# Kernel tuning notes

Measured on AMD Instinct MI355X. Metric: run time of the kernel, lower is better.

Reference implementation:

```python
import jax, jax.numpy as jnp
import numpy as np

N = 50000        # nodes
E = 800000       # edges (avg degree 16)
G = 64           # graphs in batch
F_IN = 9
OUT = 10


def setup_inputs() -> dict:
    key = jax.random.key(0)
    ks = jax.random.split(key, 20)
    def w(k, fi, fo):
        return jax.random.normal(k, (fi, fo), dtype=jnp.float32) * (1.0 / np.sqrt(fi))
    inp = {
        "x": jax.random.normal(ks[0], (N, F_IN), dtype=jnp.float32),
        "edge_index": jax.random.randint(ks[1], (2, E), 0, N, dtype=jnp.int64),
        "batch": jnp.sort(jax.random.randint(ks[2], (N,), 0, G, dtype=jnp.int64)),
        # GCNConv weights (PyG: x @ W then normalized scatter-add, + bias)
        "W1": w(ks[3], F_IN, 128), "b1": jnp.zeros((128,), jnp.float32),
        "W2": w(ks[4], 128, 256),  "b2": jnp.zeros((256,), jnp.float32),
        "W3": w(ks[5], 256, 256),  "b3": jnp.zeros((256,), jnp.float32),
        "W4": w(ks[6], 256, 256),  "b4": jnp.zeros((256,), jnp.float32),
        # dense head
        "Wl2": w(ks[7], 256, 128), "bl2": jnp.zeros((128,), jnp.float32),
        "Wl3": w(ks[8], 128, 128), "bl3": jnp.zeros((128,), jnp.float32),
        "Wl":  w(ks[9], 128, OUT), "bl":  jnp.zeros((OUT,), jnp.float32),
    }
    return inp


def reference(x, edge_index, batch, W1, b1, W2, b2, W3, b3, W4, b4,
              Wl2, bl2, Wl3, bl3, Wl, bl):
    # GCNConv with self-loops and symmetric deg^{-1/2} normalization
    loops = jnp.arange(N, dtype=edge_index.dtype)
    src = jnp.concatenate([edge_index[0], loops])   # [E+N]
    dst = jnp.concatenate([edge_index[1], loops])
    deg = jax.ops.segment_sum(jnp.ones_like(src, dtype=x.dtype), dst, num_segments=N)
    dinv = jax.lax.rsqrt(deg)                        # deg >= 1 due to self-loops
    norm = (dinv[src] * dinv[dst])[:, None]          # [E+N, 1]

    def conv(h, W, b):
        msg = (h @ W)[src] * norm                    # gather + normalize
        return jax.ops.segment_sum(msg, dst, num_segments=N) + b

    h = jax.nn.relu(conv(x, W1, b1))
    h = jax.nn.relu(conv(h, W2, b2))
    h = jax.nn.relu(conv(h, W3, b3))
    h = conv(h, W4, b4)                              # no relu before pool
    g = jax.ops.segment_max(h, batch, num_segments=G)  # global_max_pool -> [G, 256]
    g = jax.nn.relu(g @ Wl2 + bl2)
    g = jax.nn.relu(g @ Wl3 + bl3)
    out = g @ Wl + bl                                # [G, OUT]
    return jnp.squeeze(out)
```

## Files before the change

### kernel.cpp

```cpp
#include <hip/hip_runtime.h>
#include <float.h>

#define NN 50000
#define NE 800000
#define NG 64
#define CAP 64

typedef __attribute__((ext_vector_type(8))) _Float16 f16x8;
typedef __attribute__((ext_vector_type(4))) float f32x4;
typedef __attribute__((ext_vector_type(4))) _Float16 half4;
typedef __attribute__((ext_vector_type(2))) _Float16 half2v;
typedef unsigned int u32;

__device__ __forceinline__ unsigned f2mono(float f) {
  unsigned b = __float_as_uint(f);
  return (b & 0x80000000u) ? ~b : (b | 0x80000000u);
}
__device__ __forceinline__ float mono2f(unsigned u) {
  unsigned b = (u & 0x80000000u) ? (u & 0x7fffffffu) : ~u;
  return __uint_as_float(b);
}
__device__ __forceinline__ void gl_lds16(const void* g, void* l) {
  __builtin_amdgcn_global_load_lds((const __attribute__((address_space(1))) u32*)g,
                                   (__attribute__((address_space(3))) u32*)l, 16, 0, 0);
}

#define CGRID 782
#define CSTRIDE (CGRID * 256)
__global__ void k_count(const int* __restrict__ src, const int* __restrict__ dst,
                        int* __restrict__ cnt, int* __restrict__ col) {
  int idx = blockIdx.x * 256 + threadIdx.x;
#pragma unroll
  for (int k = 0; k < 4; ++k) {
    int e = idx + k * CSTRIDE;
    if (e < NE) {
      int d = dst[e];
      int s = src[e];
      if ((unsigned)d < NN && (unsigned)s < NN) {
        int pos = atomicAdd(&cnt[d], 1);
        if (pos < CAP) col[d * CAP + pos] = s;
      }
    }
  }
}

__global__ void k_dinv(const int* __restrict__ cnt, float* __restrict__ dinv,
                       const float* __restrict__ x, float* __restrict__ xs) {
  int v = blockIdx.x * blockDim.x + threadIdx.x;
  if (v >= NN) return;
  float d = rsqrtf((float)cnt[v] + 1.0f);
  dinv[v] = d;
#pragma unroll
  for (int i = 0; i < 9; ++i) xs[v * 9 + i] = x[v * 9 + i] * d;
}

__device__ __forceinline__ void splitw1(const float* W, _Float16* Wh, _Float16* Wl,
                                        int i, int K, int Nc) {
  int k = i / Nc, n = i - k * Nc;
  float w = W[i];
  _Float16 h = (_Float16)w;
  _Float16 l = (_Float16)(w - (float)h);
  Wh[(size_t)n * K + k] = h;
  Wl[(size_t)n * K + k] = l;
}
__global__ void k_splitw3(const float* __restrict__ W2, const float* __restrict__ W3,
                          const float* __restrict__ W4,
                          _Float16* __restrict__ W2h, _Float16* __restrict__ W2l,
                          _Float16* __restrict__ W3h, _Float16* __restrict__ W3l,
                          _Float16* __restrict__ W4h, _Float16* __restrict__ W4l) {
  int i = blockIdx.x * 256 + threadIdx.x;
  const int n2 = 128 * 256, n3 = 256 * 256;
  if (i < n2) splitw1(W2, W2h, W2l, i, 128, 256);
  else if (i < n2 + n3) splitw1(W3, W3h, W3l, i - n2, 256, 256);
  else if (i < n2 + 2 * n3) splitw1(W4, W4h, W4l, i - n2 - n3, 256, 256);
}

__global__ __launch_bounds__(256) void k_agg9(const float* __restrict__ xs,
                                              float* __restrict__ out,
                                              const int* __restrict__ cnt,
                                              const int* __restrict__ col,
                                              const float* __restrict__ dinv) {
  int v = (blockIdx.x * 256 + threadIdx.x) >> 4;
  int l = threadIdx.x & 15;
  if (v >= NN) return;
  int c = cnt[v]; if (c > CAP) c = CAP;
  const int* cl = col + v * CAP;
  float acc = (l < 9) ? xs[v * 9 + l] : 0.0f;
  int j = 0;
  for (; j + 4 <= c; j += 4) {
    int4 u = *(const int4*)(cl + j);
    float a0 = (l < 9) ? xs[u.x * 9 + l] : 0.f;
    float a1 = (l < 9) ? xs[u.y * 9 + l] : 0.f;
    float a2 = (l < 9) ? xs[u.z * 9 + l] : 0.f;
    float a3 = (l < 9) ? xs[u.w * 9 + l] : 0.f;
    acc += (a0 + a1) + (a2 + a3);
  }
  for (; j < c; ++j) {
    int u = cl[j];
    if (l < 9) acc += xs[u * 9 + l];
  }
  if (l < 9) out[v * 9 + l] = acc * dinv[v];
}

__global__ __launch_bounds__(256) void k_gemm9(const float* __restrict__ in,
                                               const float* __restrict__ W,
                                               const float* __restrict__ bias,
                                               const float* __restrict__ dinv,
                                               _Float16* __restrict__ out) {
  __shared__ float sW[9 * 128];
  __shared__ float sb[128];
  int t = threadIdx.x;
  if (t < 128) sb[t] = bias[t];
  for (int i = t; i < 9 * 128; i += 256) sW[i] = W[i];
  __syncthreads();
  int r = blockIdx.x * 2 + (t >> 7);
  int c = t & 127;
  if (r >= NN) return;
  float acc = sb[c];
#pragma unroll
  for (int i = 0; i < 9; ++i) acc += in[r * 9 + i] * sW[i * 128 + c];
  out[r * 128 + c] = (_Float16)(fmaxf(acc, 0.0f) * dinv[r]);
}

__global__ __launch_bounds__(256) void k_agg128(const half2v* __restrict__ h,
                                                half2v* __restrict__ out,
                                                const int* __restrict__ cnt,
                                                const int* __restrict__ col,
                                                const float* __restrict__ dinv) {
  int gw = (blockIdx.x * 256 + threadIdx.x) >> 6;
  int lane = threadIdx.x & 63;
  int w0 = gw * 2, w1 = w0 + 1;
  if (w0 >= NN) return;
  half2v s0 = h[(size_t)w0 * 64 + lane];
  half2v s1 = h[(size_t)w1 * 64 + lane];
  float a0x = (float)s0.x, a0y = (float)s0.y;
  float a1x = (float)s1.x, a1y = (float)s1.y;
  int c0 = cnt[w0]; if (c0 > CAP) c0 = CAP;
  int c1 = cnt[w1]; if (c1 > CAP) c1 = CAP;
  const int* cl0 = col + (size_t)w0 * CAP;
  const int* cl1 = col + (size_t)w1 * CAP;
  int j0 = 0, j1 = 0;
  while (j0 + 4 <= c0 && j1 + 4 <= c1) {
    int4 u0 = *(const int4*)(cl0 + j0);
    int4 u1 = *(const int4*)(cl1 + j1);
    half2v t00 = h[(size_t)u0.x * 64 + lane];
    half2v t01 = h[(size_t)u0.y * 64 + lane];
    half2v t02 = h[(size_t)u0.z * 64 + lane];
    half2v t03 = h[(size_t)u0.w * 64 + lane];
    half2v t10 = h[(size_t)u1.x * 64 + lane];
    half2v t11 = h[(size_t)u1.y * 64 + lane];
    half2v t12 = h[(size_t)u1.z * 64 + lane];
    half2v t13 = h[(size_t)u1.w * 64 + lane];
    a0x += ((float)t00.x + (float)t01.x) + ((float)t02.x + (float)t03.x);
    a0y += ((float)t00.y + (float)t01.y) + ((float)t02.y + (float)t03.y);
    a1x += ((float)t10.x + (float)t11.x) + ((float)t12.x + (float)t13.x);
    a1y += ((float)t10.y + (float)t11.y) + ((float)t12.y + (float)t13.y);
    j0 += 4; j1 += 4;
  }
  for (; j0 + 4 <= c0; j0 += 4) {
    int4 u = *(const int4*)(cl0 + j0);
    half2v t0 = h[(size_t)u.x * 64 + lane];
    half2v t1 = h[(size_t)u.y * 64 + lane];
    half2v t2 = h[(size_t)u.z * 64 + lane];
    half2v t3 = h[(size_t)u.w * 64 + lane];
    a0x += ((float)t0.x + (float)t1.x) + ((float)t2.x + (float)t3.x);
    a0y += ((float)t0.y + (float)t1.y) + ((float)t2.y + (float)t3.y);
  }
  for (; j1 + 4 <= c1; j1 += 4) {
    int4 u = *(const int4*)(cl1 + j1);
    half2v t0 = h[(size_t)u.x * 64 + lane];
    half2v t1 = h[(size_t)u.y * 64 + lane];
    half2v t2 = h[(size_t)u.z * 64 + lane];
    half2v t3 = h[(size_t)u.w * 64 + lane];
    a1x += ((float)t0.x + (float)t1.x) + ((float)t2.x + (float)t3.x);
    a1y += ((float)t0.y + (float)t1.y) + ((float)t2.y + (float)t3.y);
  }
  for (; j0 < c0; ++j0) {
    half2v tv = h[(size_t)cl0[j0] * 64 + lane];
    a0x += (float)tv.x; a0y += (float)tv.y;
  }
  for (; j1 < c1; ++j1) {
    half2v tv = h[(size_t)cl1[j1] * 64 + lane];
    a1x += (float)tv.x; a1y += (float)tv.y;
  }
  float d0 = dinv[w0], d1 = dinv[w1];
  half2v o0, o1;
  o0.x = (_Float16)(a0x * d0); o0.y = (_Float16)(a0y * d0);
  o1.x = (_Float16)(a1x * d1); o1.y = (_Float16)(a1y * d1);
  out[(size_t)w0 * 64 + lane] = o0;
  out[(size_t)w1 * 64 + lane] = o1;
}

__global__ __launch_bounds__(256) void k_agg256(const half4* __restrict__ h,
                                                half4* __restrict__ out,
                                                const int* __restrict__ cnt,
                                                const int* __restrict__ col,
                                                const float* __restrict__ dinv) {
  int gw = (blockIdx.x * 256 + threadIdx.x) >> 6;
  int lane = threadIdx.x & 63;
  int w0 = gw * 2, w1 = w0 + 1;
  if (w0 >= NN) return;
  half4 s0 = h[(size_t)w0 * 64 + lane];
  half4 s1 = h[(size_t)w1 * 64 + lane];
  float a0x = (float)s0.x, a0y = (float)s0.y, a0z = (float)s0.z, a0w = (float)s0.w;
  float a1x = (float)s1.x, a1y = (float)s1.y, a1z = (float)s1.z, a1w = (float)s1.w;
  int c0 = cnt[w0]; if (c0 > CAP) c0 = CAP;
  int c1 = cnt[w1]; if (c1 > CAP) c1 = CAP;
  const int* cl0 = col + (size_t)w0 * CAP;
  const int* cl1 = col + (size_t)w1 * CAP;
  int j0 = 0, j1 = 0;
  while (j0 + 4 <= c0 && j1 + 4 <= c1) {
    int4 u0 = *(const int4*)(cl0 + j0);
    int4 u1 = *(const int4*)(cl1 + j1);
    half4 t00 = h[(size_t)u0.x * 64 + lane];
    half4 t01 = h[(size_t)u0.y * 64 + lane];
    half4 t02 = h[(size_t)u0.z * 64 + lane];
    half4 t03 = h[(size_t)u0.w * 64 + lane];
    half4 t10 = h[(size_t)u1.x * 64 + lane];
    half4 t11 = h[(size_t)u1.y * 64 + lane];
    half4 t12 = h[(size_t)u1.z * 64 + lane];
    half4 t13 = h[(size_t)u1.w * 64 + lane];
    a0x += ((float)t00.x + (float)t01.x) + ((float)t02.x + (float)t03.x);
    a0y += ((float)t00.y + (float)t01.y) + ((float)t02.y + (float)t03.y);
    a0z += ((float)t00.z + (float)t01.z) + ((float)t02.z + (float)t03.z);
    a0w += ((float)t00.w + (float)t01.w) + ((float)t02.w + (float)t03.w);
    a1x += ((float)t10.x + (float)t11.x) + ((float)t12.x + (float)t13.x);
    a1y += ((float)t10.y + (float)t11.y) + ((float)t12.y + (float)t13.y);
    a1z += ((float)t10.z + (float)t11.z) + ((float)t12.z + (float)t13.z);
    a1w += ((float)t10.w + (float)t11.w) + ((float)t12.w + (float)t13.w);
    j0 += 4; j1 += 4;
  }
  for (; j0 + 4 <= c0; j0 += 4) {
    int4 u = *(const int4*)(cl0 + j0);
    half4 t0 = h[(size_t)u.x * 64 + lane];
    half4 t1 = h[(size_t)u.y * 64 + lane];
    half4 t2 = h[(size_t)u.z * 64 + lane];
    half4 t3 = h[(size_t)u.w * 64 + lane];
    a0x += ((float)t0.x + (float)t1.x) + ((float)t2.x + (float)t3.x);
    a0y += ((float)t0.y + (float)t1.y) + ((float)t2.y + (float)t3.y);
    a0z += ((float)t0.z + (float)t1.z) + ((float)t2.z + (float)t3.z);
    a0w += ((float)t0.w + (float)t1.w) + ((float)t2.w + (float)t3.w);
  }
  for (; j1 + 4 <= c1; j1 += 4) {
    int4 u = *(const int4*)(cl1 + j1);
    half4 t0 = h[(size_t)u.x * 64 + lane];
    half4 t1 = h[(size_t)u.y * 64 + lane];
    half4 t2 = h[(size_t)u.z * 64 + lane];
    half4 t3 = h[(size_t)u.w * 64 + lane];
    a1x += ((float)t0.x + (float)t1.x) + ((float)t2.x + (float)t3.x);
    a1y += ((float)t0.y + (float)t1.y) + ((float)t2.y + (float)t3.y);
    a1z += ((float)t0.z + (float)t1.z) + ((float)t2.z + (float)t3.z);
    a1w += ((float)t0.w + (float)t1.w) + ((float)t2.w + (float)t3.w);
  }
  for (; j0 < c0; ++j0) {
    half4 tv = h[(size_t)cl0[j0] * 64 + lane];
    a0x += (float)tv.x; a0y += (float)tv.y; a0z += (float)tv.z; a0w += (float)tv.w;
  }
  for (; j1 < c1; ++j1) {
    half4 tv = h[(size_t)cl1[j1] * 64 + lane];
    a1x += (float)tv.x; a1y += (float)tv.y; a1z += (float)tv.z; a1w += (float)tv.w;
  }
  float d0 = dinv[w0], d1 = dinv[w1];
  half4 o0, o1;
  o0.x = (_Float16)(a0x * d0); o0.y = (_Float16)(a0y * d0);
  o0.z = (_Float16)(a0z * d0); o0.w = (_Float16)(a0w * d0);
  o1.x = (_Float16)(a1x * d1); o1.y = (_Float16)(a1y * d1);
  o1.z = (_Float16)(a1z * d1); o1.w = (_Float16)(a1w * d1);
  out[(size_t)w0 * 64 + lane] = o0;
  out[(size_t)w1 * 64 + lane] = o1;
}

__global__ __launch_bounds__(256) void k_mm(const _Float16* __restrict__ A,
                                            const _Float16* __restrict__ Bh,
                                            const _Float16* __restrict__ Bl,
                                            const float* __restrict__ bias,
                                            _Float16* __restrict__ C,
                                            const float* __restrict__ dinv,
                                            const int* __restrict__ batch,
                                            unsigned* __restrict__ gpool,
                                            int M, int K, int Nc, int mode) {
  __shared__ __align__(16) _Float16 Alds[128 * 64];
  __shared__ __align__(16) _Float16 Bhl[128 * 64];
  __shared__ __align__(16) _Float16 Bll[128 * 64];
  int t = threadIdx.x;
  int wave = t >> 6, lane = t & 63;
  int wm = wave & 1, wn = wave >> 1;
  int rowBase = blockIdx.x * 128;
  int colBase = blockIdx.y * 128;
  int lm = lane & 15;
  int q  = lane >> 4;

  int srl = wave * 32 + (lane >> 3);
  int sj  = lane & 7;
  int ssw = lane >> 3;
  int gseg = sj ^ ssw;

  f32x4 acc[4][4];
#pragma unroll
  for (int i = 0; i < 4; ++i)
#pragma unroll
    for (int j = 0; j < 4; ++j) acc[i][j] = (f32x4){0.f, 0.f, 0.f, 0.f};

  int nit = K >> 6;
  for (int it = 0; it < nit; ++it) {
    __syncthreads();
#pragma unroll
    for (int c = 0; c < 4; ++c) {
      int rl = srl + c * 8;
      int ga = rowBase + rl; if (ga > M - 1) ga = M - 1;
      int gb = colBase + rl;
      unsigned off = (unsigned)it * 64 + gseg * 8;
      int ldst = (wave * 32 + c * 8) * 64 + lane * 8;
      gl_lds16(A  + (size_t)ga * K + off, Alds + ldst);
      gl_lds16(Bh + (size_t)gb * K + off, Bhl + ldst);
      gl_lds16(Bl + (size_t)gb * K + off, Bll + ldst);
    }
    __syncthreads();

#pragma unroll
    for (int s2 = 0; s2 < 2; ++s2) {
      int slotq = ((s2 << 2) | q);
      f16x8 vbh[4], vbl[4];
#pragma unroll
      for (int ni = 0; ni < 4; ++ni) {
        int rB = wn * 64 + ni * 16 + lm;
        int slot = slotq ^ (lm & 7);
        vbh[ni] = *(const f16x8*)(Bhl + rB * 64 + slot * 8);
        vbl[ni] = *(const f16x8*)(Bll + rB * 64 + slot * 8);
      }
#pragma unroll
      for (int mi = 0; mi < 4; ++mi) {
        int rA = wm * 64 + mi * 16 + lm;
        int slot = slotq ^ (lm & 7);
        f16x8 va = *(const f16x8*)(Alds + rA * 64 + slot * 8);
#pragma unroll
        for (int ni = 0; ni < 4; ++ni) {
          acc[mi][ni] = __builtin_amdgcn_mfma_f32_16x16x32_f16(va, vbh[ni], acc[mi][ni], 0, 0, 0);
          acc[mi][ni] = __builtin_amdgcn_mfma_f32_16x16x32_f16(va, vbl[ni], acc[mi][ni], 0, 0, 0);
        }
      }
    }
  }

  int rowOff = (lane >> 4) * 4;
  if (mode == 2) {
    __syncthreads();
    unsigned* ldsPool = (unsigned*)Alds;
    for (int i = t; i < 4 * 256; i += 256) ldsPool[i] = 0u;
    __syncthreads();
    int b0 = batch[rowBase];
#pragma unroll
    for (int mi = 0; mi < 4; ++mi) {
#pragma unroll
      for (int ni = 0; ni < 4; ++ni) {
        int gc = colBase + wn * 64 + ni * 16 + lm;
        float bsv = bias[gc];
#pragma unroll
        for (int r = 0; r < 4; ++r) {
          int gr = rowBase + wm * 64 + mi * 16 + rowOff + r;
          if (gr < M) {
            float v = acc[mi][ni][r] + bsv;
            int idx = batch[gr] - b0;
            if (idx < 0) idx = 0;
            if (idx > 3) idx = 3;
            atomicMax(&ldsPool[idx * 256 + gc], f2mono(v));
          }
        }
      }
    }
    __syncthreads();
#pragma unroll
    for (int s4 = 0; s4 < 4; ++s4) {
      unsigned mv = ldsPool[s4 * 256 + t];
      int gb = b0 + s4;
      if (mv && gb < NG) atomicMax(&gpool[gb * 256 + t], mv);
    }
  } else {
#pragma unroll
    for (int mi = 0; mi < 4; ++mi) {
#pragma unroll
      for (int ni = 0; ni < 4; ++ni) {
        int gc = colBase + wn * 64 + ni * 16 + lm;
        float bsv = bias[gc];
#pragma unroll
        for (int r = 0; r < 4; ++r) {
          int gr = rowBase + wm * 64 + mi * 16 + rowOff + r;
          if (gr < M) {
            float v = fmaxf(acc[mi][ni][r] + bsv, 0.0f);
            C[(size_t)gr * Nc + gc] = (_Float16)(v * dinv[gr]);
          }
        }
      }
    }
  }
}

__global__ __launch_bounds__(256) void k_head(const unsigned* __restrict__ g,
                                              const float* __restrict__ Wl2, const float* __restrict__ bl2,
                                              const float* __restrict__ Wl3, const float* __restrict__ bl3,
                                              const float* __restrict__ Wl, const float* __restrict__ bl,
                                              float* __restrict__ out) {
  __shared__ float s0[256];
  __shared__ float s1[128];
  __shared__ float s2[128];
  int b = blockIdx.x, t = threadIdx.x;
  s0[t] = mono2f(g[b * 256 + t]);
  __syncthreads();
  if (t < 128) {
    float acc = bl2[t];
    for (int k = 0; k < 256; ++k) acc += s0[k] * Wl2[k * 128 + t];
    s1[t] = fmaxf(acc, 0.0f);
  }
  __syncthreads();
  if (t < 128) {
    float acc = bl3[t];
    for (int k = 0; k < 128; ++k) acc += s1[k] * Wl3[k * 128 + t];
    s2[t] = fmaxf(acc, 0.0f);
  }
  __syncthreads();
  if (t < 10) {
    float acc = bl[t];
    for (int k = 0; k < 128; ++k) acc += s2[k] * Wl[k * 10 + t];
    out[b * 10 + t] = acc;
  }
}

extern "C" void kernel_launch(void* const* d_in, const int* in_sizes, int n_in,
                              void* d_out, int out_size, void* d_ws, size_t ws_size,
                              hipStream_t stream) {
  const float* x   = (const float*)d_in[0];
  const int* eidx  = (const int*)d_in[1];
  const int* batch = (const int*)d_in[2];
  const float* W1 = (const float*)d_in[3];   const float* b1 = (const float*)d_in[4];
  const float* W2 = (const float*)d_in[5];   const float* b2 = (const float*)d_in[6];
  const float* W3 = (const float*)d_in[7];   const float* b3 = (const float*)d_in[8];
  const float* W4 = (const float*)d_in[9];   const float* b4 = (const float*)d_in[10];
  const float* Wl2 = (const float*)d_in[11]; const float* bl2 = (const float*)d_in[12];
  const float* Wl3 = (const float*)d_in[13]; const float* bl3 = (const float*)d_in[14];
  const float* Wl  = (const float*)d_in[15]; const float* bl  = (const float*)d_in[16];
  float* out = (float*)d_out;

  _Float16* bufA = (_Float16*)d_ws;
  _Float16* bufB = bufA + (size_t)NN * 256;
  int* cnt  = (int*)(bufB + (size_t)NN * 256);
  float* dinv = (float*)(cnt + NN);
  int* col  = (int*)(dinv + NN);
  unsigned* g = (unsigned*)(col + (size_t)NN * CAP);
  _Float16* W2h = (_Float16*)(g + NG * 256);
  _Float16* W2l = W2h + 256 * 128;
  _Float16* W3h = W2l + 256 * 128;
  _Float16* W3l = W3h + 256 * 256;
  _Float16* W4h = W3l + 256 * 256;
  _Float16* W4l = W4h + 256 * 256;
  float* xs = (float*)bufA;
  float* agg9out = (float*)bufB;

  const int* src = eidx;
  const int* dst = eidx + NE;

  hipMemsetAsync(cnt, 0, NN * sizeof(int), stream);
  hipMemsetAsync(g, 0, NG * 256 * sizeof(unsigned), stream);

  k_count<<<CGRID, 256, 0, stream>>>(src, dst, cnt, col);
  k_dinv<<<(NN + 255) / 256, 256, 0, stream>>>(cnt, dinv, x, xs);

  k_splitw3<<<(128 * 256 + 2 * 256 * 256 + 255) / 256, 256, 0, stream>>>(
      W2, W3, W4, W2h, W2l, W3h, W3l, W4h, W4l);

  k_agg9<<<(NN + 15) / 16, 256, 0, stream>>>(xs, agg9out, cnt, col, dinv);
  k_gemm9<<<NN / 2, 256, 0, stream>>>(agg9out, W1, b1, dinv, bufA);

  dim3 gmm((NN + 127) / 128, 2);
  int aggGrid = ((NN / 2) * 64 + 255) / 256;

  k_agg128<<<aggGrid, 256, 0, stream>>>((const half2v*)bufA, (half2v*)bufB, cnt, col, dinv);
  k_mm<<<gmm, 256, 0, stream>>>(bufB, W2h, W2l, b2, bufA, dinv, batch, g, NN, 128, 256, 1);

  k_agg256<<<aggGrid, 256, 0, stream>>>((const half4*)bufA, (half4*)bufB, cnt, col, dinv);
  k_mm<<<gmm, 256, 0, stream>>>(bufB, W3h, W3l, b3, bufA, dinv, batch, g, NN, 256, 256, 1);

  k_agg256<<<aggGrid, 256, 0, stream>>>((const half4*)bufA, (half4*)bufB, cnt, col, dinv);
  k_mm<<<gmm, 256, 0, stream>>>(bufB, W4h, W4l, b4, bufA, dinv, batch, g, NN, 256, 256, 2);

  k_head<<<NG, 256, 0, stream>>>(g, Wl2, bl2, Wl3, bl3, Wl, bl, out);
}
```

Measured before the change: 458.1 us.

## Store adjacency indices as u16, remap GEMM block order, fold pool memset

Neighbor indices in the padded adjacency table are stored as 16-bit values instead of 32-bit, halving index traffic in every aggregation kernel. The count kernel switches to one edge per thread, the pooled-max buffer is zeroed inside k_dinv instead of by a separate memset, and the GEMM uses a 1-D grid remapped so that both column tiles of a row block run next to each other for better A-tile reuse in cache. Node ids go up to 49999, so they fit in u16, but the tail loops that still read cl[j] now read u16 values, so the change relies on that fitting.

```diff
diff --git a/kernel.cpp b/kernel.cpp
--- a/kernel.cpp
+++ b/kernel.cpp
@@ -11,6 +11,7 @@
 typedef __attribute__((ext_vector_type(4))) _Float16 half4;
 typedef __attribute__((ext_vector_type(2))) _Float16 half2v;
 typedef unsigned int u32;
+typedef unsigned short u16;
 
 __device__ __forceinline__ unsigned f2mono(float f) {
   unsigned b = __float_as_uint(f);
@@ -25,29 +26,23 @@
                                    (__attribute__((address_space(3))) u32*)l, 16, 0, 0);
 }
 
-#define CGRID 782
-#define CSTRIDE (CGRID * 256)
 __global__ void k_count(const int* __restrict__ src, const int* __restrict__ dst,
-                        int* __restrict__ cnt, int* __restrict__ col) {
-  int idx = blockIdx.x * 256 + threadIdx.x;
-#pragma unroll
-  for (int k = 0; k < 4; ++k) {
-    int e = idx + k * CSTRIDE;
-    if (e < NE) {
-      int d = dst[e];
-      int s = src[e];
-      if ((unsigned)d < NN && (unsigned)s < NN) {
-        int pos = atomicAdd(&cnt[d], 1);
-        if (pos < CAP) col[d * CAP + pos] = s;
-      }
-    }
-  }
+                        int* __restrict__ cnt, u16* __restrict__ col) {
+  int e = blockIdx.x * 256 + threadIdx.x;
+  if (e >= NE) return;
+  int d = dst[e];
+  int s = src[e];
+  if ((unsigned)d >= NN || (unsigned)s >= NN) return;
+  int pos = atomicAdd(&cnt[d], 1);
+  if (pos < CAP) col[d * CAP + pos] = (u16)s;
 }
 
 __global__ void k_dinv(const int* __restrict__ cnt, float* __restrict__ dinv,
-                       const float* __restrict__ x, float* __restrict__ xs) {
+                       const float* __restrict__ x, float* __restrict__ xs,
+                       unsigned* __restrict__ g) {
   int v = blockIdx.x * blockDim.x + threadIdx.x;
   if (v >= NN) return;
+  if (v < NG * 256) g[v] = 0u;
   float d = rsqrtf((float)cnt[v] + 1.0f);
   dinv[v] = d;
 #pragma unroll
@@ -78,21 +73,21 @@
 __global__ __launch_bounds__(256) void k_agg9(const float* __restrict__ xs,
                                               float* __restrict__ out,
                                               const int* __restrict__ cnt,
-                                              const int* __restrict__ col,
+                                              const u16* __restrict__ col,
                                               const float* __restrict__ dinv) {
   int v = (blockIdx.x * 256 + threadIdx.x) >> 4;
   int l = threadIdx.x & 15;
   if (v >= NN) return;
   int c = cnt[v]; if (c > CAP) c = CAP;
-  const int* cl = col + v * CAP;
+  const u16* cl = col + (size_t)v * CAP;
   float acc = (l < 9) ? xs[v * 9 + l] : 0.0f;
   int j = 0;
   for (; j + 4 <= c; j += 4) {
-    int4 u = *(const int4*)(cl + j);
-    float a0 = (l < 9) ? xs[u.x * 9 + l] : 0.f;
-    float a1 = (l < 9) ? xs[u.y * 9 + l] : 0.f;
-    float a2 = (l < 9) ? xs[u.z * 9 + l] : 0.f;
-    float a3 = (l < 9) ? xs[u.w * 9 + l] : 0.f;
+    ushort4 u = *(const ushort4*)(cl + j);
+    float a0 = (l < 9) ? xs[(int)u.x * 9 + l] : 0.f;
+    float a1 = (l < 9) ? xs[(int)u.y * 9 + l] : 0.f;
+    float a2 = (l < 9) ? xs[(int)u.z * 9 + l] : 0.f;
+    float a3 = (l < 9) ? xs[(int)u.w * 9 + l] : 0.f;
     acc += (a0 + a1) + (a2 + a3);
   }
   for (; j < c; ++j) {
@@ -125,7 +120,7 @@
 __global__ __launch_bounds__(256) void k_agg128(const half2v* __restrict__ h,
                                                 half2v* __restrict__ out,
                                                 const int* __restrict__ cnt,
-                                                const int* __restrict__ col,
+                                                const u16* __restrict__ col,
                                                 const float* __restrict__ dinv) {
   int gw = (blockIdx.x * 256 + threadIdx.x) >> 6;
   int lane = threadIdx.x & 63;
@@ -137,12 +132,12 @@
   float a1x = (float)s1.x, a1y = (float)s1.y;
   int c0 = cnt[w0]; if (c0 > CAP) c0 = CAP;
   int c1 = cnt[w1]; if (c1 > CAP) c1 = CAP;
-  const int* cl0 = col + (size_t)w0 * CAP;
-  const int* cl1 = col + (size_t)w1 * CAP;
+  const u16* cl0 = col + (size_t)w0 * CAP;
+  const u16* cl1 = col + (size_t)w1 * CAP;
   int j0 = 0, j1 = 0;
   while (j0 + 4 <= c0 && j1 + 4 <= c1) {
-    int4 u0 = *(const int4*)(cl0 + j0);
-    int4 u1 = *(const int4*)(cl1 + j1);
+    ushort4 u0 = *(const ushort4*)(cl0 + j0);
+    ushort4 u1 = *(const ushort4*)(cl1 + j1);
     half2v t00 = h[(size_t)u0.x * 64 + lane];
     half2v t01 = h[(size_t)u0.y * 64 + lane];
     half2v t02 = h[(size_t)u0.z * 64 + lane];
@@ -158,7 +153,7 @@
     j0 += 4; j1 += 4;
   }
   for (; j0 + 4 <= c0; j0 += 4) {
-    int4 u = *(const int4*)(cl0 + j0);
+    ushort4 u = *(const ushort4*)(cl0 + j0);
     half2v t0 = h[(size_t)u.x * 64 + lane];
     half2v t1 = h[(size_t)u.y * 64 + lane];
     half2v t2 = h[(size_t)u.z * 64 + lane];
@@ -167,7 +162,7 @@
     a0y += ((float)t0.y + (float)t1.y) + ((float)t2.y + (float)t3.y);
   }
   for (; j1 + 4 <= c1; j1 += 4) {
-    int4 u = *(const int4*)(cl1 + j1);
+    ushort4 u = *(const ushort4*)(cl1 + j1);
     half2v t0 = h[(size_t)u.x * 64 + lane];
     half2v t1 = h[(size_t)u.y * 64 + lane];
     half2v t2 = h[(size_t)u.z * 64 + lane];
@@ -194,7 +189,7 @@
 __global__ __launch_bounds__(256) void k_agg256(const half4* __restrict__ h,
                                                 half4* __restrict__ out,
                                                 const int* __restrict__ cnt,
-                                                const int* __restrict__ col,
+                                                const u16* __restrict__ col,
                                                 const float* __restrict__ dinv) {
   int gw = (blockIdx.x * 256 + threadIdx.x) >> 6;
   int lane = threadIdx.x & 63;
@@ -206,12 +201,12 @@
   float a1x = (float)s1.x, a1y = (float)s1.y, a1z = (float)s1.z, a1w = (float)s1.w;
   int c0 = cnt[w0]; if (c0 > CAP) c0 = CAP;
   int c1 = cnt[w1]; if (c1 > CAP) c1 = CAP;
-  const int* cl0 = col + (size_t)w0 * CAP;
-  const int* cl1 = col + (size_t)w1 * CAP;
+  const u16* cl0 = col + (size_t)w0 * CAP;
+  const u16* cl1 = col + (size_t)w1 * CAP;
   int j0 = 0, j1 = 0;
   while (j0 + 4 <= c0 && j1 + 4 <= c1) {
-    int4 u0 = *(const int4*)(cl0 + j0);
-    int4 u1 = *(const int4*)(cl1 + j1);
+    ushort4 u0 = *(const ushort4*)(cl0 + j0);
+    ushort4 u1 = *(const ushort4*)(cl1 + j1);
     half4 t00 = h[(size_t)u0.x * 64 + lane];
     half4 t01 = h[(size_t)u0.y * 64 + lane];
     half4 t02 = h[(size_t)u0.z * 64 + lane];
@@ -231,7 +226,7 @@
     j0 += 4; j1 += 4;
   }
   for (; j0 + 4 <= c0; j0 += 4) {
-    int4 u = *(const int4*)(cl0 + j0);
+    ushort4 u = *(const ushort4*)(cl0 + j0);
     half4 t0 = h[(size_t)u.x * 64 + lane];
     half4 t1 = h[(size_t)u.y * 64 + lane];
     half4 t2 = h[(size_t)u.z * 64 + lane];
@@ -242,7 +237,7 @@
     a0w += ((float)t0.w + (float)t1.w) + ((float)t2.w + (float)t3.w);
   }
   for (; j1 + 4 <= c1; j1 += 4) {
-    int4 u = *(const int4*)(cl1 + j1);
+    ushort4 u = *(const ushort4*)(cl1 + j1);
     half4 t0 = h[(size_t)u.x * 64 + lane];
     half4 t1 = h[(size_t)u.y * 64 + lane];
     half4 t2 = h[(size_t)u.z * 64 + lane];
@@ -282,11 +277,15 @@
   __shared__ __align__(16) _Float16 Alds[128 * 64];
   __shared__ __align__(16) _Float16 Bhl[128 * 64];
   __shared__ __align__(16) _Float16 Bll[128 * 64];
+  int bid = blockIdx.x;
+  int rblk = (bid >> 4) * 8 + (bid & 7);
+  int cblk = (bid >> 3) & 1;
+  if (rblk * 128 >= M) return;
+  int rowBase = rblk * 128;
+  int colBase = cblk * 128;
   int t = threadIdx.x;
   int wave = t >> 6, lane = t & 63;
   int wm = wave & 1, wn = wave >> 1;
-  int rowBase = blockIdx.x * 128;
-  int colBase = blockIdx.y * 128;
   int lm = lane & 15;
   int q  = lane >> 4;
 
@@ -444,7 +443,7 @@
   _Float16* bufB = bufA + (size_t)NN * 256;
   int* cnt  = (int*)(bufB + (size_t)NN * 256);
   float* dinv = (float*)(cnt + NN);
-  int* col  = (int*)(dinv + NN);
+  u16* col  = (u16*)(dinv + NN);
   unsigned* g = (unsigned*)(col + (size_t)NN * CAP);
   _Float16* W2h = (_Float16*)(g + NG * 256);
   _Float16* W2l = W2h + 256 * 128;
@@ -459,10 +458,9 @@
   const int* dst = eidx + NE;
 
   hipMemsetAsync(cnt, 0, NN * sizeof(int), stream);
-  hipMemsetAsync(g, 0, NG * 256 * sizeof(unsigned), stream);
-
-  k_count<<<CGRID, 256, 0, stream>>>(src, dst, cnt, col);
-  k_dinv<<<(NN + 255) / 256, 256, 0, stream>>>(cnt, dinv, x, xs);
+
+  k_count<<<(NE + 255) / 256, 256, 0, stream>>>(src, dst, cnt, col);
+  k_dinv<<<(NN + 255) / 256, 256, 0, stream>>>(cnt, dinv, x, xs, g);
 
   k_splitw3<<<(128 * 256 + 2 * 256 * 256 + 255) / 256, 256, 0, stream>>>(
       W2, W3, W4, W2h, W2l, W3h, W3l, W4h, W4l);
@@ -470,17 +468,17 @@
   k_agg9<<<(NN + 15) / 16, 256, 0, stream>>>(xs, agg9out, cnt, col, dinv);
   k_gemm9<<<NN / 2, 256, 0, stream>>>(agg9out, W1, b1, dinv, bufA);
 
-  dim3 gmm((NN + 127) / 128, 2);
   int aggGrid = ((NN / 2) * 64 + 255) / 256;
+  const int mmGrid = 784;
 
   k_agg128<<<aggGrid, 256, 0, stream>>>((const half2v*)bufA, (half2v*)bufB, cnt, col, dinv);
-  k_mm<<<gmm, 256, 0, stream>>>(bufB, W2h, W2l, b2, bufA, dinv, batch, g, NN, 128, 256, 1);
+  k_mm<<<mmGrid, 256, 0, stream>>>(bufB, W2h, W2l, b2, bufA, dinv, batch, g, NN, 128, 256, 1);
 
   k_agg256<<<aggGrid, 256, 0, stream>>>((const half4*)bufA, (half4*)bufB, cnt, col, dinv);
-  k_mm<<<gmm, 256, 0, stream>>>(bufB, W3h, W3l, b3, bufA, dinv, batch, g, NN, 256, 256, 1);
+  k_mm<<<mmGrid, 256, 0, stream>>>(bufB, W3h, W3l, b3, bufA, dinv, batch, g, NN, 256, 256, 1);
 
   k_agg256<<<aggGrid, 256, 0, stream>>>((const half4*)bufA, (half4*)bufB, cnt, col, dinv);
-  k_mm<<<gmm, 256, 0, stream>>>(bufB, W4h, W4l, b4, bufA, dinv, batch, g, NN, 256, 256, 2);
+  k_mm<<<mmGrid, 256, 0, stream>>>(bufB, W4h, W4l, b4, bufA, dinv, batch, g, NN, 256, 256, 2);
 
   k_head<<<NG, 256, 0, stream>>>(g, Wl2, bl2, Wl3, bl3, Wl, bl, out);
 }
```

Measured after the change: 450.9 us, median of 2. About the same (-1.6%).
